# Performance work log

Measured on AMD Instinct MI355X. Metric: run time of the kernel, lower is better.

The kernel has to match this reference:

```python
import jax, jax.numpy as jnp
import numpy as np

N_NODES = 50000
N_EDGES = 800000
IN_CH = 128
HID = 256
HEADS = 4
NEG_SLOPE = 0.2


def setup_inputs() -> dict:
    key = jax.random.key(0)
    ks = jax.random.split(key, 12)
    C1 = HID // HEADS  # 64 per head, layer 1
    inp = {
        "x": jax.random.normal(ks[0], (N_NODES, IN_CH), dtype=jnp.float32),
        "edge_index": jax.random.randint(ks[1], (2, N_EDGES), 0, N_NODES, dtype=jnp.int32),
        # layer 1: GATConv(128 -> 64, heads=4, concat=True)
        "W1": jax.random.normal(ks[2], (IN_CH, HEADS * C1), dtype=jnp.float32) * (1.0 / np.sqrt(IN_CH)),
        "a_src1": jax.random.normal(ks[3], (HEADS, C1), dtype=jnp.float32) * 0.1,
        "a_dst1": jax.random.normal(ks[4], (HEADS, C1), dtype=jnp.float32) * 0.1,
        "b1": jnp.zeros((HEADS * C1,), dtype=jnp.float32),
        # layer 2: GATConv(256 -> 256, heads=1, concat=False)
        "W2": jax.random.normal(ks[5], (HID, HID), dtype=jnp.float32) * (1.0 / np.sqrt(HID)),
        "a_src2": jax.random.normal(ks[6], (1, HID), dtype=jnp.float32) * 0.1,
        "a_dst2": jax.random.normal(ks[7], (1, HID), dtype=jnp.float32) * 0.1,
        "b2": jnp.zeros((HID,), dtype=jnp.float32),
    }
    return inp


def _gat_conv(x, src, dst, W, a_src, a_dst, H, C, n_nodes):
    """One PyG-style GATConv (eval mode, self-loops already appended)."""
    h = (x @ W).reshape(n_nodes, H, C)                      # [N,H,C]
    alpha_src = jnp.sum(h * a_src[None], axis=-1)           # [N,H]
    alpha_dst = jnp.sum(h * a_dst[None], axis=-1)           # [N,H]
    e = jax.nn.leaky_relu(alpha_src[src] + alpha_dst[dst], NEG_SLOPE)  # [E,H]
    # segment softmax over incoming edges of each dst node
    m = jax.ops.segment_max(e, dst, num_segments=n_nodes)  # [N,H]
    e = jnp.exp(e - m[dst])
    denom = jax.ops.segment_sum(e, dst, num_segments=n_nodes)
    alpha = e / (denom[dst] + 1e-16)                        # [E,H]
    msg = h[src] * alpha[:, :, None]                        # [E,H,C]
    return jax.ops.segment_sum(msg, dst, num_segments=n_nodes)  # [N,H,C]


def reference(x, edge_index, W1, a_src1, a_dst1, b1, W2, a_src2, a_dst2, b2):
    n = x.shape[0]
    loops = jnp.arange(n, dtype=edge_index.dtype)
    src = jnp.concatenate([edge_index[0], loops])
    dst = jnp.concatenate([edge_index[1], loops])
    C1 = HID // HEADS
    # layer 1: heads=4, concat -> [N, HID], then ELU (dropout inactive at eval)
    h1 = _gat_conv(x, src, dst, W1, a_src1, a_dst1, HEADS, C1, n)
    h1 = jax.nn.elu(h1.reshape(n, HEADS * C1) + b1)
    # layer 2: heads=1, concat=False -> mean over heads (trivial for H=1)
    h2 = _gat_conv(h1, src, dst, W2, a_src2, a_dst2, 1, HID, n)
    return h2.reshape(n, HID) + b2
```

## Files before the change

### kernel.cpp

```cpp
#include <hip/hip_runtime.h>
#include <hip/hip_fp16.h>

#define NNODES 50000
#define NEDGES 800000
#define HIDDIM 256
#define EN (NEDGES + NNODES)

constexpr float NEG = 0.2f;

typedef __attribute__((ext_vector_type(8))) short short8_t;
typedef __attribute__((ext_vector_type(4))) float floatx4;

__device__ __forceinline__ float lrelu(float v){ return v >= 0.f ? v : NEG*v; }

__device__ __forceinline__ unsigned short bf16_rn(float x){
  unsigned u = __float_as_uint(x);
  return (unsigned short)((u + 0x7FFFu + ((u >> 16) & 1u)) >> 16);
}

__device__ __forceinline__ float4 ldh4(const __half* p){
  union { float2 f; __half2 h[2]; } u;
  u.f = *reinterpret_cast<const float2*>(p);
  const float2 lo = __half22float2(u.h[0]);
  const float2 hi = __half22float2(u.h[1]);
  return make_float4(lo.x, lo.y, hi.x, hi.y);
}

__global__ void k_init_counts(int* counts, int n){
  int i = blockIdx.x*blockDim.x + threadIdx.x;
  if (i < n) counts[i] = 1;
}
__global__ void k_count(const int* __restrict__ ei, int* counts, int E){
  int e = blockIdx.x*blockDim.x + threadIdx.x;
  if (e < E) atomicAdd(&counts[ei[E + e]], 1);
}

#define SCAN_CHUNK 2048
__global__ __launch_bounds__(256) void k_scan_a(const int* __restrict__ counts,
                                                int* __restrict__ bsum, int n){
  __shared__ int ws[4];
  const int t = threadIdx.x;
  const int idx0 = blockIdx.x*SCAN_CHUNK + t*8;
  int s = 0;
  #pragma unroll
  for (int i = 0; i < 8; ++i) if (idx0 + i < n) s += counts[idx0 + i];
  for (int off = 32; off; off >>= 1) s += __shfl_xor(s, off);
  if ((t & 63) == 0) ws[t >> 6] = s;
  __syncthreads();
  if (t == 0) bsum[blockIdx.x] = ws[0] + ws[1] + ws[2] + ws[3];
}
__global__ void k_scan_b(const int* __restrict__ bsum, int* __restrict__ boff,
                         int* __restrict__ offs, int nb, int n){
  if (threadIdx.x == 0){
    int run = 0;
    for (int i = 0; i < nb; ++i){ boff[i] = run; run += bsum[i]; }
    offs[n] = run;
  }
}
__global__ __launch_bounds__(256) void k_scan_c(const int* __restrict__ counts,
                                                const int* __restrict__ boff,
                                                int* __restrict__ offs,
                                                int* __restrict__ cursor, int n){
  __shared__ int sc[256];
  const int t = threadIdx.x;
  const int idx0 = blockIdx.x*SCAN_CHUNK + t*8;
  int v[8], pre[8], s = 0;
  #pragma unroll
  for (int i = 0; i < 8; ++i){
    v[i] = (idx0 + i < n) ? counts[idx0 + i] : 0;
    pre[i] = s; s += v[i];
  }
  sc[t] = s;
  __syncthreads();
  int run = s;
  for (int off = 1; off < 256; off <<= 1){
    int add = (t >= off) ? sc[t - off] : 0;
    __syncthreads();
    sc[t] += add;
    __syncthreads();
  }
  const int excl = sc[t] - run;
  const int toff = boff[blockIdx.x] + excl;
  #pragma unroll
  for (int i = 0; i < 8; ++i){
    if (idx0 + i < n){
      const int o = toff + pre[i];
      offs[idx0 + i] = o;
      cursor[idx0 + i] = o;
    }
  }
}
__global__ void k_scatter(const int* __restrict__ ei, int* cursor,
                          int* __restrict__ esrc, int E, int n){
  int e = blockIdx.x*blockDim.x + threadIdx.x;
  if (e < E){
    int s = ei[e], d = ei[E+e];
    esrc[atomicAdd(&cursor[d], 1)] = s;
  } else if (e < E + n){
    int i = e - E;
    esrc[atomicAdd(&cursor[i], 1)] = i;
  }
}

__global__ void k_splitW(const float* __restrict__ W, unsigned short* __restrict__ hi,
                         unsigned short* __restrict__ lo, int K){
  int idx = blockIdx.x*256 + threadIdx.x;
  if (idx >= K*HIDDIM) return;
  int k = idx / HIDDIM, n = idx % HIDDIM;
  float w = W[idx];
  unsigned short h = bf16_rn(w);
  float hf = __uint_as_float((unsigned)h << 16);
  unsigned short l = bf16_rn(w - hf);
  int p = ((k >> 3)*HIDDIM + n)*8 + (k & 7);
  hi[p] = h; lo[p] = l;
}

template<int K, int NH>
__global__ __launch_bounds__(256) void k_gemm_mfma(
    const float* __restrict__ A,
    const unsigned short* __restrict__ Bhi, const unsigned short* __restrict__ Blo,
    const float* __restrict__ aS, const float* __restrict__ aD,
    __half* __restrict__ Hout, float* __restrict__ as_o, float* __restrict__ ad_o, int M)
{
  constexpr int LDSK = K + 8;
  __shared__ unsigned short sAhi[64*LDSK];
  __shared__ unsigned short sAlo[64*LDSK];
  __shared__ float lred_s[64][4], lred_d[64][4];
  const int tid = threadIdx.x;
  const int row0 = blockIdx.x*64;

  constexpr int CH = 64*K/4/256;
  #pragma unroll
  for (int c = 0; c < CH; ++c){
    const int chunk = c*256 + tid;
    const int r = chunk/(K/4), ko = (chunk%(K/4))*4;
    const int gr = min(row0 + r, M-1);
    const float4 v = *reinterpret_cast<const float4*>(A + (size_t)gr*K + ko);
    ushort4 h, l;
    h.x = bf16_rn(v.x); l.x = bf16_rn(v.x - __uint_as_float((unsigned)h.x<<16));
    h.y = bf16_rn(v.y); l.y = bf16_rn(v.y - __uint_as_float((unsigned)h.y<<16));
    h.z = bf16_rn(v.z); l.z = bf16_rn(v.z - __uint_as_float((unsigned)h.z<<16));
    h.w = bf16_rn(v.w); l.w = bf16_rn(v.w - __uint_as_float((unsigned)h.w<<16));
    *reinterpret_cast<ushort4*>(&sAhi[r*LDSK + ko]) = h;
    *reinterpret_cast<ushort4*>(&sAlo[r*LDSK + ko]) = l;
  }
  __syncthreads();

  const int w = tid >> 6, l = tid & 63;
  const int lr = l & 15, lg = l >> 4;
  const int n0 = w*64;
  floatx4 acc[4][4] = {};

  for (int ks = 0; ks < K/32; ++ks){
    short8_t ah[4], al[4], bh[4], bl[4];
    #pragma unroll
    for (int m = 0; m < 4; ++m){
      const int off = (16*m + lr)*LDSK + ks*32 + lg*8;
      ah[m] = *reinterpret_cast<const short8_t*>(&sAhi[off]);
      al[m] = *reinterpret_cast<const short8_t*>(&sAlo[off]);
    }
    #pragma unroll
    for (int n = 0; n < 4; ++n){
      const int boff = (((ks*4 + lg)*HIDDIM) + n0 + 16*n + lr)*8;
      bh[n] = *reinterpret_cast<const short8_t*>(&Bhi[boff]);
      bl[n] = *reinterpret_cast<const short8_t*>(&Blo[boff]);
    }
    #pragma unroll
    for (int m = 0; m < 4; ++m)
      #pragma unroll
      for (int n = 0; n < 4; ++n){
        acc[m][n] = __builtin_amdgcn_mfma_f32_16x16x32_bf16(ah[m], bh[n], acc[m][n], 0,0,0);
        acc[m][n] = __builtin_amdgcn_mfma_f32_16x16x32_bf16(ah[m], bl[n], acc[m][n], 0,0,0);
        acc[m][n] = __builtin_amdgcn_mfma_f32_16x16x32_bf16(al[m], bh[n], acc[m][n], 0,0,0);
      }
  }

  #pragma unroll
  for (int m = 0; m < 4; ++m){
    #pragma unroll
    for (int r = 0; r < 4; ++r){
      const int row = row0 + 16*m + lg*4 + r;
      if (row < M){
        #pragma unroll
        for (int n = 0; n < 4; ++n)
          Hout[(size_t)row*HIDDIM + n0 + 16*n + lr] = __float2half(acc[m][n][r]);
      }
    }
  }

  float asv[4], adv_[4];
  #pragma unroll
  for (int n = 0; n < 4; ++n){ asv[n] = aS[n0+16*n+lr]; adv_[n] = aD[n0+16*n+lr]; }
  #pragma unroll
  for (int m = 0; m < 4; ++m){
    #pragma unroll
    for (int r = 0; r < 4; ++r){
      float ps = 0.f, pd = 0.f;
      #pragma unroll
      for (int n = 0; n < 4; ++n){
        ps = fmaf(acc[m][n][r], asv[n], ps);
        pd = fmaf(acc[m][n][r], adv_[n], pd);
      }
      #pragma unroll
      for (int off = 1; off <= 8; off <<= 1){
        ps += __shfl_xor(ps, off);
        pd += __shfl_xor(pd, off);
      }
      const int rloc = 16*m + lg*4 + r;
      if (NH == 4){
        if (lr == 0 && row0 + rloc < M){
          as_o[(row0+rloc)*4 + w] = ps;
          ad_o[(row0+rloc)*4 + w] = pd;
        }
      } else {
        if (lr == 0){ lred_s[rloc][w] = ps; lred_d[rloc][w] = pd; }
      }
    }
  }
  if (NH == 1){
    __syncthreads();
    if (tid < 64 && row0 + tid < M){
      float a = lred_s[tid][0]+lred_s[tid][1]+lred_s[tid][2]+lred_s[tid][3];
      float b = lred_d[tid][0]+lred_d[tid][1]+lred_d[tid][2]+lred_d[tid][3];
      as_o[row0+tid] = a; ad_o[row0+tid] = b;
    }
  }
}

template<int NH>
__global__ __launch_bounds__(256) void k_prep(
    const float* __restrict__ as_, const float* __restrict__ ad_,
    const int* __restrict__ offs, const int* __restrict__ esrc,
    __half* __restrict__ p16, int n)
{
  const int lane = threadIdx.x & 63;
  const int node = blockIdx.x*4 + (threadIdx.x >> 6);
  if (node >= n) return;
  const int start = offs[node], end = offs[node+1];

  float adv[NH], m[NH], dsum[NH];
  #pragma unroll
  for (int h = 0; h < NH; ++h){ adv[h] = ad_[node*NH + h]; m[h] = -1e30f; dsum[h] = 0.f; }

  for (int e = start + lane; e < end; e += 64){
    const int s = esrc[e];
    if (NH == 4){
      const float4 av = *reinterpret_cast<const float4*>(as_ + (size_t)s*4);
      const float a[4] = {av.x, av.y, av.z, av.w};
      #pragma unroll
      for (int h = 0; h < 4; ++h){
        const float v = lrelu(a[h] + adv[h]);
        const float mo = m[h], mn = fmaxf(mo, v);
        dsum[h] = dsum[h]*__expf(mo - mn) + __expf(v - mn);
        m[h] = mn;
      }
    } else {
      const float v = lrelu(as_[s] + adv[0]);
      const float mo = m[0], mn = fmaxf(mo, v);
      dsum[0] = dsum[0]*__expf(mo - mn) + __expf(v - mn);
      m[0] = mn;
    }
  }
  #pragma unroll
  for (int h = 0; h < NH; ++h){
    for (int off = 32; off; off >>= 1){
      const float mo = __shfl_xor(m[h], off);
      const float dd = __shfl_xor(dsum[h], off);
      const float mn = fmaxf(m[h], mo);
      dsum[h] = dsum[h]*__expf(m[h] - mn) + dd*__expf(mo - mn);
      m[h] = mn;
    }
  }
  float rd[NH];
  #pragma unroll
  for (int h = 0; h < NH; ++h) rd[h] = 1.f/(dsum[h] + 1e-16f);

  for (int e = start + lane; e < end; e += 64){
    const int s = esrc[e];
    if (NH == 4){
      const float4 av = *reinterpret_cast<const float4*>(as_ + (size_t)s*4);
      const float a[4] = {av.x, av.y, av.z, av.w};
      union { float2 f; __half2 h2[2]; } o;
      o.h2[0] = __half2{__float2half(__expf(lrelu(a[0] + adv[0]) - m[0]) * rd[0]),
                        __float2half(__expf(lrelu(a[1] + adv[1]) - m[1]) * rd[1])};
      o.h2[1] = __half2{__float2half(__expf(lrelu(a[2] + adv[2]) - m[2]) * rd[2]),
                        __float2half(__expf(lrelu(a[3] + adv[3]) - m[3]) * rd[3])};
      *reinterpret_cast<float2*>(&p16[(size_t)4*e]) = o.f;
    } else {
      const float p = __expf(lrelu(as_[s] + adv[0]) - m[0]) * rd[0];
      p16[e] = __float2half(p);
    }
  }
}

template<int NH, bool DO_ELU>
__global__ __launch_bounds__(256) void k_agg3(
    const __half* __restrict__ Hs, const __half* __restrict__ p16,
    const int* __restrict__ offs, const int* __restrict__ esrc,
    const float* __restrict__ bias, float* __restrict__ Out, int n)
{
  const int lane = threadIdx.x & 63;
  const int node = blockIdx.x*4 + (threadIdx.x >> 6);
  if (node >= n) return;
  const int start = offs[node], end = offs[node+1];
  const int head = (NH == 4) ? (lane >> 4) : 0;
  const __half* hp = Hs + 4*lane;

  float4 a0 = {0,0,0,0}, a1 = {0,0,0,0}, a2 = {0,0,0,0}, a3 = {0,0,0,0};
  int e = start;
  for (; e + 4 <= end; e += 4){
    const int s0 = esrc[e+0], s1 = esrc[e+1], s2 = esrc[e+2], s3 = esrc[e+3];
    const float p0 = __half2float(p16[(size_t)NH*(e+0) + head]);
    const float p1 = __half2float(p16[(size_t)NH*(e+1) + head]);
    const float p2 = __half2float(p16[(size_t)NH*(e+2) + head]);
    const float p3 = __half2float(p16[(size_t)NH*(e+3) + head]);
    const float4 h0 = ldh4(hp + (size_t)s0*HIDDIM);
    const float4 h1 = ldh4(hp + (size_t)s1*HIDDIM);
    const float4 h2 = ldh4(hp + (size_t)s2*HIDDIM);
    const float4 h3 = ldh4(hp + (size_t)s3*HIDDIM);
    a0.x = fmaf(p0, h0.x, a0.x); a0.y = fmaf(p0, h0.y, a0.y);
    a0.z = fmaf(p0, h0.z, a0.z); a0.w = fmaf(p0, h0.w, a0.w);
    a1.x = fmaf(p1, h1.x, a1.x); a1.y = fmaf(p1, h1.y, a1.y);
    a1.z = fmaf(p1, h1.z, a1.z); a1.w = fmaf(p1, h1.w, a1.w);
    a2.x = fmaf(p2, h2.x, a2.x); a2.y = fmaf(p2, h2.y, a2.y);
    a2.z = fmaf(p2, h2.z, a2.z); a2.w = fmaf(p2, h2.w, a2.w);
    a3.x = fmaf(p3, h3.x, a3.x); a3.y = fmaf(p3, h3.y, a3.y);
    a3.z = fmaf(p3, h3.z, a3.z); a3.w = fmaf(p3, h3.w, a3.w);
  }
  for (; e < end; ++e){
    const int s = esrc[e];
    const float p = __half2float(p16[(size_t)NH*e + head]);
    const float4 hv = ldh4(hp + (size_t)s*HIDDIM);
    a0.x = fmaf(p, hv.x, a0.x); a0.y = fmaf(p, hv.y, a0.y);
    a0.z = fmaf(p, hv.z, a0.z); a0.w = fmaf(p, hv.w, a0.w);
  }
  float4 acc;
  acc.x = (a0.x + a1.x) + (a2.x + a3.x);
  acc.y = (a0.y + a1.y) + (a2.y + a3.y);
  acc.z = (a0.z + a1.z) + (a2.z + a3.z);
  acc.w = (a0.w + a1.w) + (a2.w + a3.w);

  const float4 bv = *reinterpret_cast<const float4*>(bias + 4*lane);
  acc.x += bv.x; acc.y += bv.y; acc.z += bv.z; acc.w += bv.w;
  if (DO_ELU){
    acc.x = acc.x > 0.f ? acc.x : __expf(acc.x) - 1.f;
    acc.y = acc.y > 0.f ? acc.y : __expf(acc.y) - 1.f;
    acc.z = acc.z > 0.f ? acc.z : __expf(acc.z) - 1.f;
    acc.w = acc.w > 0.f ? acc.w : __expf(acc.w) - 1.f;
  }
  *reinterpret_cast<float4*>(Out + (size_t)node*HIDDIM + 4*lane) = acc;
}

extern "C" void kernel_launch(void* const* d_in, const int* in_sizes, int n_in,
                              void* d_out, int out_size, void* d_ws, size_t ws_size,
                              hipStream_t stream)
{
  const float* x    = (const float*)d_in[0];
  const int*   ei   = (const int*)  d_in[1];
  const float* W1   = (const float*)d_in[2];
  const float* aS1  = (const float*)d_in[3];
  const float* aD1  = (const float*)d_in[4];
  const float* b1   = (const float*)d_in[5];
  const float* W2   = (const float*)d_in[6];
  const float* aS2  = (const float*)d_in[7];
  const float* aD2  = (const float*)d_in[8];
  const float* b2   = (const float*)d_in[9];
  float* out = (float*)d_out;

  char* ws = (char*)d_ws;
  size_t off = 0;
  auto alloc = [&](size_t bytes){ void* p = ws + off; off += (bytes + 255) & ~255ull; return p; };
  __half* hbuf  = (__half*)alloc((size_t)NNODES*HIDDIM*sizeof(__half));
  __half* p16   = (__half*)alloc((size_t)4*EN*sizeof(__half));
  float* as1    = (float*)alloc((size_t)NNODES*4*sizeof(float));
  float* ad1    = (float*)alloc((size_t)NNODES*4*sizeof(float));
  float* as2    = (float*)alloc((size_t)NNODES*sizeof(float));
  float* ad2    = (float*)alloc((size_t)NNODES*sizeof(float));
  unsigned short* W1hi = (unsigned short*)alloc((size_t)128*HIDDIM*sizeof(short));
  unsigned short* W1lo = (unsigned short*)alloc((size_t)128*HIDDIM*sizeof(short));
  unsigned short* W2hi = (unsigned short*)alloc((size_t)256*HIDDIM*sizeof(short));
  unsigned short* W2lo = (unsigned short*)alloc((size_t)256*HIDDIM*sizeof(short));
  int*   counts = (int*)alloc((size_t)NNODES*sizeof(int));
  int*   offs   = (int*)alloc((size_t)(NNODES+1)*sizeof(int));
  int*   cursor = (int*)alloc((size_t)NNODES*sizeof(int));
  int*   bsum   = (int*)alloc(64*sizeof(int));
  int*   boff   = (int*)alloc(64*sizeof(int));
  int*   esrc   = (int*)alloc((size_t)EN*sizeof(int));

  const int nscan = (NNODES + SCAN_CHUNK - 1)/SCAN_CHUNK;

  k_init_counts<<<(NNODES+255)/256, 256, 0, stream>>>(counts, NNODES);
  k_count     <<<(NEDGES+255)/256, 256, 0, stream>>>(ei, counts, NEDGES);
  k_scan_a    <<<nscan, 256, 0, stream>>>(counts, bsum, NNODES);
  k_scan_b    <<<1, 64, 0, stream>>>(bsum, boff, offs, nscan, NNODES);
  k_scan_c    <<<nscan, 256, 0, stream>>>(counts, boff, offs, cursor, NNODES);
  k_scatter   <<<(EN+255)/256, 256, 0, stream>>>(ei, cursor, esrc, NEDGES, NNODES);

  k_splitW<<<(128*HIDDIM+255)/256, 256, 0, stream>>>(W1, W1hi, W1lo, 128);
  k_splitW<<<(256*HIDDIM+255)/256, 256, 0, stream>>>(W2, W2hi, W2lo, 256);

  const int gemm_grid = (NNODES + 63)/64;
  const int node_grid = (NNODES + 3)/4;

  k_gemm_mfma<128,4><<<gemm_grid, 256, 0, stream>>>(x, W1hi, W1lo, aS1, aD1, hbuf, as1, ad1, NNODES);
  k_prep<4><<<node_grid, 256, 0, stream>>>(as1, ad1, offs, esrc, p16, NNODES);
  k_agg3<4,true><<<node_grid, 256, 0, stream>>>(hbuf, p16, offs, esrc, b1, out, NNODES);

  k_gemm_mfma<256,1><<<gemm_grid, 256, 0, stream>>>(out, W2hi, W2lo, aS2, aD2, hbuf, as2, ad2, NNODES);
  k_prep<1><<<node_grid, 256, 0, stream>>>(as2, ad2, offs, esrc, p16, NNODES);
  k_agg3<1,false><<<node_grid, 256, 0, stream>>>(hbuf, p16, offs, esrc, b2, out, NNODES);
}
```

Before: 351.4 us.

## Pre-split GEMM A operands into tiled bf16 hi/lo layout, fused into aggregation epilogue

The GEMM no longer converts fp32 A rows to bf16 hi/lo pairs in LDS. It reads A fragments directly from global memory in a pre-tiled MFMA-friendly layout. For layer 2, the layer-1 aggregation kernel writes its ELU output straight into that split tiled format, so the fp32 intermediate is never written or re-read. For layer 1, a new k_splitA kernel converts x up front, which adds a launch and an extra pass over x. The A-side LDS and its sync are removed, and the layer-2 A traffic is halved in bytes. In exchange, A fragment loads now come from global/L2 instead of LDS.

After: 365.7 us. 4.1% more time.

```diff
diff --git a/kernel.cpp b/kernel.cpp
--- a/kernel.cpp
+++ b/kernel.cpp
@@ -5,6 +5,7 @@
 #define NEDGES 800000
 #define HIDDIM 256
 #define EN (NEDGES + NNODES)
+#define NTILES ((NNODES + 63)/64)
 
 constexpr float NEG = 0.2f;
 
@@ -115,49 +116,48 @@
   hi[p] = h; lo[p] = l;
 }
 
+__global__ __launch_bounds__(256) void k_splitA(const float* __restrict__ X,
+                                                unsigned short* __restrict__ hi,
+                                                unsigned short* __restrict__ lo,
+                                                int M, int K){
+  const int idx = blockIdx.x*256 + threadIdx.x;
+  if (idx >= M*(K/4)) return;
+  const int r = idx/(K/4), kq = idx%(K/4);
+  const float4 v = *reinterpret_cast<const float4*>(X + (size_t)r*K + kq*4);
+  ushort4 h, l;
+  h.x = bf16_rn(v.x); l.x = bf16_rn(v.x - __uint_as_float((unsigned)h.x<<16));
+  h.y = bf16_rn(v.y); l.y = bf16_rn(v.y - __uint_as_float((unsigned)h.y<<16));
+  h.z = bf16_rn(v.z); l.z = bf16_rn(v.z - __uint_as_float((unsigned)h.z<<16));
+  h.w = bf16_rn(v.w); l.w = bf16_rn(v.w - __uint_as_float((unsigned)h.w<<16));
+  const size_t o = ((size_t)(r>>6)*(K/8) + (kq>>1))*512 + (r&63)*8 + (kq&1)*4;
+  *reinterpret_cast<ushort4*>(hi + o) = h;
+  *reinterpret_cast<ushort4*>(lo + o) = l;
+}
+
 template<int K, int NH>
 __global__ __launch_bounds__(256) void k_gemm_mfma(
-    const float* __restrict__ A,
+    const unsigned short* __restrict__ Ahi, const unsigned short* __restrict__ Alo,
     const unsigned short* __restrict__ Bhi, const unsigned short* __restrict__ Blo,
     const float* __restrict__ aS, const float* __restrict__ aD,
     __half* __restrict__ Hout, float* __restrict__ as_o, float* __restrict__ ad_o, int M)
 {
-  constexpr int LDSK = K + 8;
-  __shared__ unsigned short sAhi[64*LDSK];
-  __shared__ unsigned short sAlo[64*LDSK];
   __shared__ float lred_s[64][4], lred_d[64][4];
   const int tid = threadIdx.x;
-  const int row0 = blockIdx.x*64;
-
-  constexpr int CH = 64*K/4/256;
-  #pragma unroll
-  for (int c = 0; c < CH; ++c){
-    const int chunk = c*256 + tid;
-    const int r = chunk/(K/4), ko = (chunk%(K/4))*4;
-    const int gr = min(row0 + r, M-1);
-    const float4 v = *reinterpret_cast<const float4*>(A + (size_t)gr*K + ko);
-    ushort4 h, l;
-    h.x = bf16_rn(v.x); l.x = bf16_rn(v.x - __uint_as_float((unsigned)h.x<<16));
-    h.y = bf16_rn(v.y); l.y = bf16_rn(v.y - __uint_as_float((unsigned)h.y<<16));
-    h.z = bf16_rn(v.z); l.z = bf16_rn(v.z - __uint_as_float((unsigned)h.z<<16));
-    h.w = bf16_rn(v.w); l.w = bf16_rn(v.w - __uint_as_float((unsigned)h.w<<16));
-    *reinterpret_cast<ushort4*>(&sAhi[r*LDSK + ko]) = h;
-    *reinterpret_cast<ushort4*>(&sAlo[r*LDSK + ko]) = l;
-  }
-  __syncthreads();
-
   const int w = tid >> 6, l = tid & 63;
   const int lr = l & 15, lg = l >> 4;
+  const int row0 = blockIdx.x*64;
   const int n0 = w*64;
   floatx4 acc[4][4] = {};
 
+  const size_t abase = (size_t)blockIdx.x*(K/8)*512 + (size_t)lr*8;
+
   for (int ks = 0; ks < K/32; ++ks){
     short8_t ah[4], al[4], bh[4], bl[4];
+    const size_t ao = abase + (size_t)(ks*4 + lg)*512;
     #pragma unroll
     for (int m = 0; m < 4; ++m){
-      const int off = (16*m + lr)*LDSK + ks*32 + lg*8;
-      ah[m] = *reinterpret_cast<const short8_t*>(&sAhi[off]);
-      al[m] = *reinterpret_cast<const short8_t*>(&sAlo[off]);
+      ah[m] = *reinterpret_cast<const short8_t*>(&Ahi[ao + m*128]);
+      al[m] = *reinterpret_cast<const short8_t*>(&Alo[ao + m*128]);
     }
     #pragma unroll
     for (int n = 0; n < 4; ++n){
@@ -293,11 +293,12 @@
   }
 }
 
-template<int NH, bool DO_ELU>
+template<int NH, bool DO_ELU, bool SPLIT_OUT>
 __global__ __launch_bounds__(256) void k_agg3(
     const __half* __restrict__ Hs, const __half* __restrict__ p16,
     const int* __restrict__ offs, const int* __restrict__ esrc,
-    const float* __restrict__ bias, float* __restrict__ Out, int n)
+    const float* __restrict__ bias, float* __restrict__ Out,
+    unsigned short* __restrict__ Ohi, unsigned short* __restrict__ Olo, int n)
 {
   const int lane = threadIdx.x & 63;
   const int node = blockIdx.x*4 + (threadIdx.x >> 6);
@@ -348,7 +349,18 @@
     acc.z = acc.z > 0.f ? acc.z : __expf(acc.z) - 1.f;
     acc.w = acc.w > 0.f ? acc.w : __expf(acc.w) - 1.f;
   }
-  *reinterpret_cast<float4*>(Out + (size_t)node*HIDDIM + 4*lane) = acc;
+  if (SPLIT_OUT){
+    ushort4 h, l;
+    h.x = bf16_rn(acc.x); l.x = bf16_rn(acc.x - __uint_as_float((unsigned)h.x<<16));
+    h.y = bf16_rn(acc.y); l.y = bf16_rn(acc.y - __uint_as_float((unsigned)h.y<<16));
+    h.z = bf16_rn(acc.z); l.z = bf16_rn(acc.z - __uint_as_float((unsigned)h.z<<16));
+    h.w = bf16_rn(acc.w); l.w = bf16_rn(acc.w - __uint_as_float((unsigned)h.w<<16));
+    const size_t o = ((size_t)(node>>6)*32 + (lane>>1))*512 + (node&63)*8 + (lane&1)*4;
+    *reinterpret_cast<ushort4*>(Ohi + o) = h;
+    *reinterpret_cast<ushort4*>(Olo + o) = l;
+  } else {
+    *reinterpret_cast<float4*>(Out + (size_t)node*HIDDIM + 4*lane) = acc;
+  }
 }
 
 extern "C" void kernel_launch(void* const* d_in, const int* in_sizes, int n_in,
@@ -370,6 +382,14 @@
   char* ws = (char*)d_ws;
   size_t off = 0;
   auto alloc = [&](size_t bytes){ void* p = ws + off; off += (bytes + 255) & ~255ull; return p; };
+
+  const size_t tshorts1 = (size_t)NTILES*16*512;
+  const size_t tshorts2 = (size_t)NTILES*32*512;
+
+  unsigned short* h1hi = (unsigned short*)alloc(tshorts2*sizeof(short));
+  unsigned short* h1lo = (unsigned short*)alloc(tshorts2*sizeof(short));
+  unsigned short* xhi  = h1hi;
+  unsigned short* xlo  = h1hi + tshorts1;
   __half* hbuf  = (__half*)alloc((size_t)NNODES*HIDDIM*sizeof(__half));
   __half* p16   = (__half*)alloc((size_t)4*EN*sizeof(__half));
   float* as1    = (float*)alloc((size_t)NNODES*4*sizeof(float));
@@ -398,15 +418,16 @@
 
   k_splitW<<<(128*HIDDIM+255)/256, 256, 0, stream>>>(W1, W1hi, W1lo, 128);
   k_splitW<<<(256*HIDDIM+255)/256, 256, 0, stream>>>(W2, W2hi, W2lo, 256);
-
-  const int gemm_grid = (NNODES + 63)/64;
+  k_splitA<<<(NNODES*(128/4)+255)/256, 256, 0, stream>>>(x, xhi, xlo, NNODES, 128);
+
+  const int gemm_grid = NTILES;
   const int node_grid = (NNODES + 3)/4;
 
-  k_gemm_mfma<128,4><<<gemm_grid, 256, 0, stream>>>(x, W1hi, W1lo, aS1, aD1, hbuf, as1, ad1, NNODES);
+  k_gemm_mfma<128,4><<<gemm_grid, 256, 0, stream>>>(xhi, xlo, W1hi, W1lo, aS1, aD1, hbuf, as1, ad1, NNODES);
   k_prep<4><<<node_grid, 256, 0, stream>>>(as1, ad1, offs, esrc, p16, NNODES);
-  k_agg3<4,true><<<node_grid, 256, 0, stream>>>(hbuf, p16, offs, esrc, b1, out, NNODES);
-
-  k_gemm_mfma<256,1><<<gemm_grid, 256, 0, stream>>>(out, W2hi, W2lo, aS2, aD2, hbuf, as2, ad2, NNODES);
+  k_agg3<4,true,true><<<node_grid, 256, 0, stream>>>(hbuf, p16, offs, esrc, b1, nullptr, h1hi, h1lo, NNODES);
+
+  k_gemm_mfma<256,1><<<gemm_grid, 256, 0, stream>>>(h1hi, h1lo, W2hi, W2lo, aS2, aD2, hbuf, as2, ad2, NNODES);
   k_prep<1><<<node_grid, 256, 0, stream>>>(as2, ad2, offs, esrc, p16, NNODES);
-  k_agg3<1,false><<<node_grid, 256, 0, stream>>>(hbuf, p16, offs, esrc, b2, out, NNODES);
-}
+  k_agg3<1,false,false><<<node_grid, 256, 0, stream>>>(hbuf, p16, offs, esrc, b2, out, nullptr, nullptr, NNODES);
+}
```

## Aggregate before transform in both GAT layers and fold attention vectors into weights

Applied to the files above, without the earlier changes.

Precomputes W·a_src and W·a_dst so attention logits come straight from x, without first forming h = xW. Both layers now aggregate the narrower raw features first (128-wide fp16 x per head in layer 1, 256-wide fp16 h1 in layer 2) and apply the GEMM afterwards. Bias, ELU and the layer-2 logits are fused into the layer-1 GEMM epilogue. The aggregated features are fed to the MFMA as a single bf16 term instead of a hi/lo split, and x is rounded to fp16 before aggregation, so precision is lower than the previous three-product split.

New measurement: 387.8 us. +10.4%, slower.

```diff
diff --git a/kernel.cpp b/kernel.cpp
--- a/kernel.cpp
+++ b/kernel.cpp
@@ -5,6 +5,8 @@
 #define NEDGES 800000
 #define HIDDIM 256
 #define EN (NEDGES + NNODES)
+#define NTILES ((NNODES + 63)/64)
+#define NT64 (NTILES*64)
 
 constexpr float NEG = 0.2f;
 
@@ -115,115 +117,64 @@
   hi[p] = h; lo[p] = l;
 }
 
-template<int K, int NH>
-__global__ __launch_bounds__(256) void k_gemm_mfma(
-    const float* __restrict__ A,
-    const unsigned short* __restrict__ Bhi, const unsigned short* __restrict__ Blo,
-    const float* __restrict__ aS, const float* __restrict__ aD,
-    __half* __restrict__ Hout, float* __restrict__ as_o, float* __restrict__ ad_o, int M)
-{
-  constexpr int LDSK = K + 8;
-  __shared__ unsigned short sAhi[64*LDSK];
-  __shared__ unsigned short sAlo[64*LDSK];
-  __shared__ float lred_s[64][4], lred_d[64][4];
-  const int tid = threadIdx.x;
-  const int row0 = blockIdx.x*64;
-
-  constexpr int CH = 64*K/4/256;
-  #pragma unroll
-  for (int c = 0; c < CH; ++c){
-    const int chunk = c*256 + tid;
-    const int r = chunk/(K/4), ko = (chunk%(K/4))*4;
-    const int gr = min(row0 + r, M-1);
-    const float4 v = *reinterpret_cast<const float4*>(A + (size_t)gr*K + ko);
-    ushort4 h, l;
-    h.x = bf16_rn(v.x); l.x = bf16_rn(v.x - __uint_as_float((unsigned)h.x<<16));
-    h.y = bf16_rn(v.y); l.y = bf16_rn(v.y - __uint_as_float((unsigned)h.y<<16));
-    h.z = bf16_rn(v.z); l.z = bf16_rn(v.z - __uint_as_float((unsigned)h.z<<16));
-    h.w = bf16_rn(v.w); l.w = bf16_rn(v.w - __uint_as_float((unsigned)h.w<<16));
-    *reinterpret_cast<ushort4*>(&sAhi[r*LDSK + ko]) = h;
-    *reinterpret_cast<ushort4*>(&sAlo[r*LDSK + ko]) = l;
-  }
-  __syncthreads();
-
-  const int w = tid >> 6, l = tid & 63;
-  const int lr = l & 15, lg = l >> 4;
-  const int n0 = w*64;
-  floatx4 acc[4][4] = {};
-
-  for (int ks = 0; ks < K/32; ++ks){
-    short8_t ah[4], al[4], bh[4], bl[4];
-    #pragma unroll
-    for (int m = 0; m < 4; ++m){
-      const int off = (16*m + lr)*LDSK + ks*32 + lg*8;
-      ah[m] = *reinterpret_cast<const short8_t*>(&sAhi[off]);
-      al[m] = *reinterpret_cast<const short8_t*>(&sAlo[off]);
-    }
-    #pragma unroll
-    for (int n = 0; n < 4; ++n){
-      const int boff = (((ks*4 + lg)*HIDDIM) + n0 + 16*n + lr)*8;
-      bh[n] = *reinterpret_cast<const short8_t*>(&Bhi[boff]);
-      bl[n] = *reinterpret_cast<const short8_t*>(&Blo[boff]);
-    }
-    #pragma unroll
-    for (int m = 0; m < 4; ++m)
-      #pragma unroll
-      for (int n = 0; n < 4; ++n){
-        acc[m][n] = __builtin_amdgcn_mfma_f32_16x16x32_bf16(ah[m], bh[n], acc[m][n], 0,0,0);
-        acc[m][n] = __builtin_amdgcn_mfma_f32_16x16x32_bf16(ah[m], bl[n], acc[m][n], 0,0,0);
-        acc[m][n] = __builtin_amdgcn_mfma_f32_16x16x32_bf16(al[m], bh[n], acc[m][n], 0,0,0);
-      }
-  }
-
-  #pragma unroll
-  for (int m = 0; m < 4; ++m){
-    #pragma unroll
-    for (int r = 0; r < 4; ++r){
-      const int row = row0 + 16*m + lg*4 + r;
-      if (row < M){
-        #pragma unroll
-        for (int n = 0; n < 4; ++n)
-          Hout[(size_t)row*HIDDIM + n0 + 16*n + lr] = __float2half(acc[m][n][r]);
-      }
-    }
-  }
-
-  float asv[4], adv_[4];
-  #pragma unroll
-  for (int n = 0; n < 4; ++n){ asv[n] = aS[n0+16*n+lr]; adv_[n] = aD[n0+16*n+lr]; }
-  #pragma unroll
-  for (int m = 0; m < 4; ++m){
-    #pragma unroll
-    for (int r = 0; r < 4; ++r){
-      float ps = 0.f, pd = 0.f;
-      #pragma unroll
-      for (int n = 0; n < 4; ++n){
-        ps = fmaf(acc[m][n][r], asv[n], ps);
-        pd = fmaf(acc[m][n][r], adv_[n], pd);
-      }
-      #pragma unroll
-      for (int off = 1; off <= 8; off <<= 1){
-        ps += __shfl_xor(ps, off);
-        pd += __shfl_xor(pd, off);
-      }
-      const int rloc = 16*m + lg*4 + r;
-      if (NH == 4){
-        if (lr == 0 && row0 + rloc < M){
-          as_o[(row0+rloc)*4 + w] = ps;
-          ad_o[(row0+rloc)*4 + w] = pd;
-        }
-      } else {
-        if (lr == 0){ lred_s[rloc][w] = ps; lred_d[rloc][w] = pd; }
-      }
-    }
-  }
-  if (NH == 1){
-    __syncthreads();
-    if (tid < 64 && row0 + tid < M){
-      float a = lred_s[tid][0]+lred_s[tid][1]+lred_s[tid][2]+lred_s[tid][3];
-      float b = lred_d[tid][0]+lred_d[tid][1]+lred_d[tid][2]+lred_d[tid][3];
-      as_o[row0+tid] = a; ad_o[row0+tid] = b;
-    }
+__global__ void k_va(const float* __restrict__ W1, const float* __restrict__ aS1,
+                     const float* __restrict__ aD1, const float* __restrict__ W2,
+                     const float* __restrict__ aS2, const float* __restrict__ aD2,
+                     float* __restrict__ va1, float* __restrict__ va2){
+  const int t = threadIdx.x;
+  if (t < 128){
+    #pragma unroll
+    for (int h = 0; h < 4; ++h){
+      float s = 0.f, d = 0.f;
+      for (int k = 0; k < 64; ++k){
+        const float w = W1[t*HIDDIM + h*64 + k];
+        s = fmaf(w, aS1[h*64 + k], s);
+        d = fmaf(w, aD1[h*64 + k], d);
+      }
+      va1[t*8 + h] = s;
+      va1[t*8 + 4 + h] = d;
+    }
+  } else {
+    for (int c = t - 128; c < 256; c += 128){
+      float s = 0.f, d = 0.f;
+      for (int j = 0; j < 256; ++j){
+        const float w = W2[c*HIDDIM + j];
+        s = fmaf(w, aS2[j], s);
+        d = fmaf(w, aD2[j], d);
+      }
+      va2[c*2] = s; va2[c*2+1] = d;
+    }
+  }
+}
+
+__global__ __launch_bounds__(256) void k_xh_logits(
+    const float* __restrict__ X, const float* __restrict__ va1,
+    __half* __restrict__ xh, float* __restrict__ as1, float* __restrict__ ad1, int n)
+{
+  const int lane = threadIdx.x & 63;
+  const int node = blockIdx.x*4 + (threadIdx.x >> 6);
+  if (node >= n) return;
+  const float2 xv = *reinterpret_cast<const float2*>(X + (size_t)node*128 + 2*lane);
+  *reinterpret_cast<__half2*>(xh + (size_t)node*128 + 2*lane) = __float22half2_rn(xv);
+
+  const float4 vs0 = *reinterpret_cast<const float4*>(va1 + (2*lane)*8);
+  const float4 vd0 = *reinterpret_cast<const float4*>(va1 + (2*lane)*8 + 4);
+  const float4 vs1 = *reinterpret_cast<const float4*>(va1 + (2*lane+1)*8);
+  const float4 vd1 = *reinterpret_cast<const float4*>(va1 + (2*lane+1)*8 + 4);
+  float ps[4], pd[4];
+  ps[0] = xv.x*vs0.x + xv.y*vs1.x;  pd[0] = xv.x*vd0.x + xv.y*vd1.x;
+  ps[1] = xv.x*vs0.y + xv.y*vs1.y;  pd[1] = xv.x*vd0.y + xv.y*vd1.y;
+  ps[2] = xv.x*vs0.z + xv.y*vs1.z;  pd[2] = xv.x*vd0.z + xv.y*vd1.z;
+  ps[3] = xv.x*vs0.w + xv.y*vs1.w;  pd[3] = xv.x*vd0.w + xv.y*vd1.w;
+  #pragma unroll
+  for (int h = 0; h < 4; ++h)
+    for (int off = 32; off; off >>= 1){
+      ps[h] += __shfl_xor(ps[h], off);
+      pd[h] += __shfl_xor(pd[h], off);
+    }
+  if (lane == 0){
+    *reinterpret_cast<float4*>(as1 + (size_t)node*4) = make_float4(ps[0],ps[1],ps[2],ps[3]);
+    *reinterpret_cast<float4*>(ad1 + (size_t)node*4) = make_float4(pd[0],pd[1],pd[2],pd[3]);
   }
 }
 
@@ -293,27 +244,154 @@
   }
 }
 
-template<int NH, bool DO_ELU>
-__global__ __launch_bounds__(256) void k_agg3(
-    const __half* __restrict__ Hs, const __half* __restrict__ p16,
+__global__ __launch_bounds__(256) void k_agg1(
+    const __half* __restrict__ xh, const __half* __restrict__ p16,
     const int* __restrict__ offs, const int* __restrict__ esrc,
-    const float* __restrict__ bias, float* __restrict__ Out, int n)
+    unsigned short* __restrict__ xagg, int n)
 {
   const int lane = threadIdx.x & 63;
   const int node = blockIdx.x*4 + (threadIdx.x >> 6);
   if (node >= n) return;
   const int start = offs[node], end = offs[node+1];
-  const int head = (NH == 4) ? (lane >> 4) : 0;
+  const __half* hp = xh + 2*lane;
+
+  float ax[4] = {0,0,0,0}, ay[4] = {0,0,0,0};
+  int e = start;
+  for (; e + 8 <= end; e += 8){
+    int s[8]; float2 pv[8]; unsigned xv[8];
+    #pragma unroll
+    for (int i = 0; i < 8; ++i) s[i] = esrc[e+i];
+    #pragma unroll
+    for (int i = 0; i < 8; ++i) pv[i] = *reinterpret_cast<const float2*>(p16 + (size_t)4*(e+i));
+    #pragma unroll
+    for (int i = 0; i < 8; ++i) xv[i] = *reinterpret_cast<const unsigned*>(hp + (size_t)s[i]*128);
+    #pragma unroll
+    for (int i = 0; i < 8; ++i){
+      union { unsigned u; __half2 h; } ux; ux.u = xv[i];
+      const float2 xf = __half22float2(ux.h);
+      union { float2 f; __half2 h2[2]; } up; up.f = pv[i];
+      const float2 p01 = __half22float2(up.h2[0]);
+      const float2 p23 = __half22float2(up.h2[1]);
+      ax[0] = fmaf(p01.x, xf.x, ax[0]); ay[0] = fmaf(p01.x, xf.y, ay[0]);
+      ax[1] = fmaf(p01.y, xf.x, ax[1]); ay[1] = fmaf(p01.y, xf.y, ay[1]);
+      ax[2] = fmaf(p23.x, xf.x, ax[2]); ay[2] = fmaf(p23.x, xf.y, ay[2]);
+      ax[3] = fmaf(p23.y, xf.x, ax[3]); ay[3] = fmaf(p23.y, xf.y, ay[3]);
+    }
+  }
+  for (; e < end; ++e){
+    const int s = esrc[e];
+    union { unsigned u; __half2 h; } ux;
+    ux.u = *reinterpret_cast<const unsigned*>(hp + (size_t)s*128);
+    const float2 xf = __half22float2(ux.h);
+    union { float2 f; __half2 h2[2]; } up;
+    up.f = *reinterpret_cast<const float2*>(p16 + (size_t)4*e);
+    const float2 p01 = __half22float2(up.h2[0]);
+    const float2 p23 = __half22float2(up.h2[1]);
+    ax[0] = fmaf(p01.x, xf.x, ax[0]); ay[0] = fmaf(p01.x, xf.y, ay[0]);
+    ax[1] = fmaf(p01.y, xf.x, ax[1]); ay[1] = fmaf(p01.y, xf.y, ay[1]);
+    ax[2] = fmaf(p23.x, xf.x, ax[2]); ay[2] = fmaf(p23.x, xf.y, ay[2]);
+    ax[3] = fmaf(p23.y, xf.x, ax[3]); ay[3] = fmaf(p23.y, xf.y, ay[3]);
+  }
+  #pragma unroll
+  for (int h = 0; h < 4; ++h){
+    const unsigned pk = (unsigned)bf16_rn(ax[h]) | ((unsigned)bf16_rn(ay[h]) << 16);
+    *reinterpret_cast<unsigned*>(xagg + (size_t)node*512 + h*128 + 2*lane) = pk;
+  }
+}
+
+__global__ __launch_bounds__(256) void k_gemm1(
+    const unsigned short* __restrict__ Xagg,
+    const unsigned short* __restrict__ Bhi, const unsigned short* __restrict__ Blo,
+    const float* __restrict__ b1, const float* __restrict__ va2,
+    __half* __restrict__ h1e, float* __restrict__ as2, float* __restrict__ ad2, int M)
+{
+  __shared__ float lred_s[64][4], lred_d[64][4];
+  const int tid = threadIdx.x;
+  const int w = tid >> 6, l = tid & 63;
+  const int lr = l & 15, lg = l >> 4;
+  const int row0 = blockIdx.x*64;
+  const int n0 = w*64;
+  floatx4 acc[4][4] = {};
+
+  for (int ks = 0; ks < 4; ++ks){
+    short8_t a_[4], bh[4], bl[4];
+    #pragma unroll
+    for (int m = 0; m < 4; ++m){
+      const size_t ao = (size_t)(row0 + 16*m + lr)*512 + w*128 + ks*32 + lg*8;
+      a_[m] = *reinterpret_cast<const short8_t*>(&Xagg[ao]);
+    }
+    #pragma unroll
+    for (int n = 0; n < 4; ++n){
+      const int boff = (((ks*4 + lg)*HIDDIM) + n0 + 16*n + lr)*8;
+      bh[n] = *reinterpret_cast<const short8_t*>(&Bhi[boff]);
+      bl[n] = *reinterpret_cast<const short8_t*>(&Blo[boff]);
+    }
+    #pragma unroll
+    for (int m = 0; m < 4; ++m)
+      #pragma unroll
+      for (int n = 0; n < 4; ++n){
+        acc[m][n] = __builtin_amdgcn_mfma_f32_16x16x32_bf16(a_[m], bh[n], acc[m][n], 0,0,0);
+        acc[m][n] = __builtin_amdgcn_mfma_f32_16x16x32_bf16(a_[m], bl[n], acc[m][n], 0,0,0);
+      }
+  }
+
+  float bcol[4], v2s[4], v2d[4];
+  #pragma unroll
+  for (int n = 0; n < 4; ++n){
+    const int col = n0 + 16*n + lr;
+    bcol[n] = b1[col];
+    v2s[n] = va2[col*2];
+    v2d[n] = va2[col*2+1];
+  }
+  #pragma unroll
+  for (int m = 0; m < 4; ++m){
+    #pragma unroll
+    for (int r = 0; r < 4; ++r){
+      const int row = row0 + 16*m + lg*4 + r;
+      float ps = 0.f, pd = 0.f;
+      #pragma unroll
+      for (int n = 0; n < 4; ++n){
+        float v = acc[m][n][r] + bcol[n];
+        v = v > 0.f ? v : __expf(v) - 1.f;
+        if (row < M) h1e[(size_t)row*HIDDIM + n0 + 16*n + lr] = __float2half(v);
+        ps = fmaf(v, v2s[n], ps);
+        pd = fmaf(v, v2d[n], pd);
+      }
+      #pragma unroll
+      for (int off = 1; off <= 8; off <<= 1){
+        ps += __shfl_xor(ps, off);
+        pd += __shfl_xor(pd, off);
+      }
+      const int rloc = 16*m + lg*4 + r;
+      if (lr == 0){ lred_s[rloc][w] = ps; lred_d[rloc][w] = pd; }
+    }
+  }
+  __syncthreads();
+  if (tid < 64 && row0 + tid < M){
+    as2[row0+tid] = lred_s[tid][0]+lred_s[tid][1]+lred_s[tid][2]+lred_s[tid][3];
+    ad2[row0+tid] = lred_d[tid][0]+lred_d[tid][1]+lred_d[tid][2]+lred_d[tid][3];
+  }
+}
+
+__global__ __launch_bounds__(256) void k_agg2(
+    const __half* __restrict__ Hs, const __half* __restrict__ p16,
+    const int* __restrict__ offs, const int* __restrict__ esrc,
+    unsigned short* __restrict__ xagg2, int n)
+{
+  const int lane = threadIdx.x & 63;
+  const int node = blockIdx.x*4 + (threadIdx.x >> 6);
+  if (node >= n) return;
+  const int start = offs[node], end = offs[node+1];
   const __half* hp = Hs + 4*lane;
 
   float4 a0 = {0,0,0,0}, a1 = {0,0,0,0}, a2 = {0,0,0,0}, a3 = {0,0,0,0};
   int e = start;
   for (; e + 4 <= end; e += 4){
     const int s0 = esrc[e+0], s1 = esrc[e+1], s2 = esrc[e+2], s3 = esrc[e+3];
-    const float p0 = __half2float(p16[(size_t)NH*(e+0) + head]);
-    const float p1 = __half2float(p16[(size_t)NH*(e+1) + head]);
-    const float p2 = __half2float(p16[(size_t)NH*(e+2) + head]);
-    const float p3 = __half2float(p16[(size_t)NH*(e+3) + head]);
+    const float p0 = __half2float(p16[e+0]);
+    const float p1 = __half2float(p16[e+1]);
+    const float p2 = __half2float(p16[e+2]);
+    const float p3 = __half2float(p16[e+3]);
     const float4 h0 = ldh4(hp + (size_t)s0*HIDDIM);
     const float4 h1 = ldh4(hp + (size_t)s1*HIDDIM);
     const float4 h2 = ldh4(hp + (size_t)s2*HIDDIM);
@@ -329,7 +407,7 @@
   }
   for (; e < end; ++e){
     const int s = esrc[e];
-    const float p = __half2float(p16[(size_t)NH*e + head]);
+    const float p = __half2float(p16[e]);
     const float4 hv = ldh4(hp + (size_t)s*HIDDIM);
     a0.x = fmaf(p, hv.x, a0.x); a0.y = fmaf(p, hv.y, a0.y);
     a0.z = fmaf(p, hv.z, a0.z); a0.w = fmaf(p, hv.w, a0.w);
@@ -340,15 +418,61 @@
   acc.z = (a0.z + a1.z) + (a2.z + a3.z);
   acc.w = (a0.w + a1.w) + (a2.w + a3.w);
 
-  const float4 bv = *reinterpret_cast<const float4*>(bias + 4*lane);
-  acc.x += bv.x; acc.y += bv.y; acc.z += bv.z; acc.w += bv.w;
-  if (DO_ELU){
-    acc.x = acc.x > 0.f ? acc.x : __expf(acc.x) - 1.f;
-    acc.y = acc.y > 0.f ? acc.y : __expf(acc.y) - 1.f;
-    acc.z = acc.z > 0.f ? acc.z : __expf(acc.z) - 1.f;
-    acc.w = acc.w > 0.f ? acc.w : __expf(acc.w) - 1.f;
-  }
-  *reinterpret_cast<float4*>(Out + (size_t)node*HIDDIM + 4*lane) = acc;
+  uint2 pk;
+  pk.x = (unsigned)bf16_rn(acc.x) | ((unsigned)bf16_rn(acc.y) << 16);
+  pk.y = (unsigned)bf16_rn(acc.z) | ((unsigned)bf16_rn(acc.w) << 16);
+  *reinterpret_cast<uint2*>(xagg2 + (size_t)node*HIDDIM + 4*lane) = pk;
+}
+
+__global__ __launch_bounds__(256) void k_gemm2(
+    const unsigned short* __restrict__ Xagg2,
+    const unsigned short* __restrict__ Bhi, const unsigned short* __restrict__ Blo,
+    const float* __restrict__ b2, float* __restrict__ Out, int M)
+{
+  const int tid = threadIdx.x;
+  const int w = tid >> 6, l = tid & 63;
+  const int lr = l & 15, lg = l >> 4;
+  const int row0 = blockIdx.x*64;
+  const int n0 = w*64;
+  floatx4 acc[4][4] = {};
+
+  for (int ks = 0; ks < 8; ++ks){
+    short8_t a_[4], bh[4], bl[4];
+    #pragma unroll
+    for (int m = 0; m < 4; ++m){
+      const size_t ao = (size_t)(row0 + 16*m + lr)*HIDDIM + ks*32 + lg*8;
+      a_[m] = *reinterpret_cast<const short8_t*>(&Xagg2[ao]);
+    }
+    #pragma unroll
+    for (int n = 0; n < 4; ++n){
+      const int boff = (((ks*4 + lg)*HIDDIM) + n0 + 16*n + lr)*8;
+      bh[n] = *reinterpret_cast<const short8_t*>(&Bhi[boff]);
+      bl[n] = *reinterpret_cast<const short8_t*>(&Blo[boff]);
+    }
+    #pragma unroll
+    for (int m = 0; m < 4; ++m)
+      #pragma unroll
+      for (int n = 0; n < 4; ++n){
+        acc[m][n] = __builtin_amdgcn_mfma_f32_16x16x32_bf16(a_[m], bh[n], acc[m][n], 0,0,0);
+        acc[m][n] = __builtin_amdgcn_mfma_f32_16x16x32_bf16(a_[m], bl[n], acc[m][n], 0,0,0);
+      }
+  }
+
+  float bcol[4];
+  #pragma unroll
+  for (int n = 0; n < 4; ++n) bcol[n] = b2[n0 + 16*n + lr];
+  #pragma unroll
+  for (int m = 0; m < 4; ++m){
+    #pragma unroll
+    for (int r = 0; r < 4; ++r){
+      const int row = row0 + 16*m + lg*4 + r;
+      if (row < M){
+        #pragma unroll
+        for (int n = 0; n < 4; ++n)
+          Out[(size_t)row*HIDDIM + n0 + 16*n + lr] = acc[m][n][r] + bcol[n];
+      }
+    }
+  }
 }
 
 extern "C" void kernel_launch(void* const* d_in, const int* in_sizes, int n_in,
@@ -370,12 +494,18 @@
   char* ws = (char*)d_ws;
   size_t off = 0;
   auto alloc = [&](size_t bytes){ void* p = ws + off; off += (bytes + 255) & ~255ull; return p; };
-  __half* hbuf  = (__half*)alloc((size_t)NNODES*HIDDIM*sizeof(__half));
+
+  unsigned short* xagg  = (unsigned short*)alloc((size_t)NT64*512*sizeof(short));
+  __half*         h1e   = (__half*)alloc((size_t)NT64*HIDDIM*sizeof(__half));
+  unsigned short* xagg2 = (unsigned short*)alloc((size_t)NT64*HIDDIM*sizeof(short));
+  __half*         xh    = (__half*)xagg2;
   __half* p16   = (__half*)alloc((size_t)4*EN*sizeof(__half));
   float* as1    = (float*)alloc((size_t)NNODES*4*sizeof(float));
   float* ad1    = (float*)alloc((size_t)NNODES*4*sizeof(float));
   float* as2    = (float*)alloc((size_t)NNODES*sizeof(float));
   float* ad2    = (float*)alloc((size_t)NNODES*sizeof(float));
+  float* va1    = (float*)alloc(128*8*sizeof(float));
+  float* va2    = (float*)alloc(256*2*sizeof(float));
   unsigned short* W1hi = (unsigned short*)alloc((size_t)128*HIDDIM*sizeof(short));
   unsigned short* W1lo = (unsigned short*)alloc((size_t)128*HIDDIM*sizeof(short));
   unsigned short* W2hi = (unsigned short*)alloc((size_t)256*HIDDIM*sizeof(short));
@@ -388,6 +518,7 @@
   int*   esrc   = (int*)alloc((size_t)EN*sizeof(int));
 
   const int nscan = (NNODES + SCAN_CHUNK - 1)/SCAN_CHUNK;
+  const int node_grid = (NNODES + 3)/4;
 
   k_init_counts<<<(NNODES+255)/256, 256, 0, stream>>>(counts, NNODES);
   k_count     <<<(NEDGES+255)/256, 256, 0, stream>>>(ei, counts, NEDGES);
@@ -396,17 +527,16 @@
   k_scan_c    <<<nscan, 256, 0, stream>>>(counts, boff, offs, cursor, NNODES);
   k_scatter   <<<(EN+255)/256, 256, 0, stream>>>(ei, cursor, esrc, NEDGES, NNODES);
 
+  k_va<<<1, 256, 0, stream>>>(W1, aS1, aD1, W2, aS2, aD2, va1, va2);
   k_splitW<<<(128*HIDDIM+255)/256, 256, 0, stream>>>(W1, W1hi, W1lo, 128);
   k_splitW<<<(256*HIDDIM+255)/256, 256, 0, stream>>>(W2, W2hi, W2lo, 256);
-
-  const int gemm_grid = (NNODES + 63)/64;
-  const int node_grid = (NNODES + 3)/4;
-
-  k_gemm_mfma<128,4><<<gemm_grid, 256, 0, stream>>>(x, W1hi, W1lo, aS1, aD1, hbuf, as1, ad1, NNODES);
+  k_xh_logits<<<node_grid, 256, 0, stream>>>(x, va1, xh, as1, ad1, NNODES);
+
   k_prep<4><<<node_grid, 256, 0, stream>>>(as1, ad1, offs, esrc, p16, NNODES);
-  k_agg3<4,true><<<node_grid, 256, 0, stream>>>(hbuf, p16, offs, esrc, b1, out, NNODES);
-
-  k_gemm_mfma<256,1><<<gemm_grid, 256, 0, stream>>>(out, W2hi, W2lo, aS2, aD2, hbuf, as2, ad2, NNODES);
+  k_agg1<<<node_grid, 256, 0, stream>>>(xh, p16, offs, esrc, xagg, NNODES);
+  k_gemm1<<<NTILES, 256, 0, stream>>>(xagg, W1hi, W1lo, b1, va2, h1e, as2, ad2, NNODES);
+
   k_prep<1><<<node_grid, 256, 0, stream>>>(as2, ad2, offs, esrc, p16, NNODES);
-  k_agg3<1,false><<<node_grid, 256, 0, stream>>>(hbuf, p16, offs, esrc, b2, out, NNODES);
-}
+  k_agg2<<<node_grid, 256, 0, stream>>>(h1e, p16, offs, esrc, xagg2, NNODES);
+  k_gemm2<<<NTILES, 256, 0, stream>>>(xagg2, W2hi, W2lo, b2, out, NNODES);
+}
```
